# Performance work log

Measured on AMD Instinct MI355X. Metric: run time of the kernel, lower is better.

The kernel has to match this reference:

```python
import jax, jax.numpy as jnp
import numpy as np

S_IN = 32      # input spatial size
KSZ = 3        # kernel size
STRIDE = 1
S_OUT = (S_IN - KSZ) // STRIDE + 1   # 30
C_IN = 16      # input capsule types
C_OUT = 32     # output capsule types
ROUTINGS = 3
EPS = 1e-7     # K.epsilon()


def _child_parent_map(size_in, size_out, kernel_size):
    # For each parent position, the flat indices of its kernel_size^2 children.
    cpm = np.zeros((size_out ** 2, kernel_size ** 2), dtype=np.int32)
    for p in range(size_out ** 2):
        idx = []
        for kr in range(kernel_size):
            start = kr * size_in + p % size_out + (p // size_out) * size_in
            idx.extend(range(start, start + kernel_size))
        cpm[p] = idx
    return cpm

_CPM = jnp.asarray(_child_parent_map(S_IN, S_OUT, KSZ))  # [S_OUT^2, KSZ^2]


def setup_inputs() -> dict:
    key = jax.random.key(0)
    k1, k2, k3, k4, k5 = jax.random.split(key, 5)
    return {
        "input_act": jax.random.uniform(k1, (S_IN, S_IN, C_IN, 1), dtype=jnp.float32),
        "input_pose": jax.random.normal(k2, (S_IN, S_IN, C_IN, 4, 4), dtype=jnp.float32),
        "transformation_weights": jax.random.normal(k3, (1, KSZ * KSZ * C_IN, C_OUT, 4, 4), dtype=jnp.float32) * 0.1,
        "beta_a": jax.random.normal(k4, (1, 1, C_OUT), dtype=jnp.float32),
        "beta_v": jax.random.normal(k5, (1, 1, C_OUT, 1), dtype=jnp.float32),
    }


def reference(input_act, input_pose, transformation_weights, beta_a, beta_v):
    P = S_OUT ** 2                 # parent positions
    N = KSZ * KSZ * C_IN           # children per parent

    pose = input_pose.reshape(S_IN ** 2, C_IN, 4, 4)
    act = input_act.reshape(S_IN ** 2, C_IN, 1)

    # gather children per parent position (irregular gather via child_parent_map)
    pose_f = pose[_CPM].reshape(P, N, 4, 4)        # [P, N, 4, 4]
    act_f = act[_CPM].reshape(P, N, 1, 1)          # [P, N, 1, 1] (broadcasts over C_OUT)

    W = transformation_weights[0]                  # [N, C_OUT, 4, 4]
    # votes[p,n,c,i,j] = sum_k pose_f[p,n,i,k] * W[n,c,k,j] (avoids K.tile materialization)
    votes = jnp.einsum('pnik,nckj->pncij', pose_f, W).reshape(P, N, C_OUT, 16)

    rr = jnp.full((P, N, C_OUT, 1), 1.0 / C_OUT, dtype=votes.dtype)

    out_act = None
    means = None
    for i in range(ROUTINGS):
        lambd = 0.01 * (1.0 - 0.95 ** i)
        # ---- M step ----
        rs = jnp.sum(rr, axis=1, keepdims=True)                              # [P,1,C,1]
        means = jnp.sum(rr * votes, axis=1, keepdims=True) / rs              # [P,1,C,16]
        var = jnp.sum(rr * jnp.square(votes - means), axis=1, keepdims=True) / rs
        std = jnp.sqrt(var)                                                  # [P,1,C,16]
        costs = beta_v + jnp.log(std + EPS) * rs                             # [P,1,C,16]
        out_act = jax.nn.sigmoid(lambd * (beta_a - jnp.sum(costs, axis=-1)))[..., None]  # [P,1,C,1]
        if i < ROUTINGS - 1:
            # ---- E step ----
            prob_exp = -jnp.sum(jnp.square(votes - means) / (2.0 * jnp.square(std)),
                                axis=-1, keepdims=True)                      # [P,N,C,1]
            prob_main = -jnp.sum(jnp.log(std + EPS), axis=-1, keepdims=True)  # [P,1,C,1]
            zz = jnp.log(out_act + EPS) + prob_main + prob_exp
            rr = jax.nn.softmax(zz, axis=0)                                   # softmax over parent axis, as in source

    out_act = out_act.reshape(S_OUT, S_OUT, C_OUT, 1)
    out_pose = means.reshape(S_OUT, S_OUT, C_OUT, 4, 4)
    return (out_act, out_pose)
```

## Files before the change

### kernel.cpp

```cpp
#include <hip/hip_runtime.h>
#include <hip/hip_bf16.h>


#define S_IN   32
#define S_OUT  30
#define PP     (S_OUT * S_OUT)
#define NN     144
#define NPO    113
#define EPSF   1e-7f
#define CLAMPA 80.0f

template <bool FIRST, bool LAST>
__global__ __launch_bounds__(256, 2) void mstep_kernel(
    const float* __restrict__ pose,
    const float* __restrict__ W,
    const float* __restrict__ beta_a,
    const float* __restrict__ beta_v,
    const float* __restrict__ colsum,
    float* __restrict__ zero0,
    float* __restrict__ zero1,
    float* __restrict__ meanw,
    float* __restrict__ i2vw,
    float* __restrict__ basew,
    float* __restrict__ out,
    float lambd)
{
    const int p = blockIdx.x;
    const int t = threadIdx.x;
    const int c = t & 31;
    const int slot = t >> 5;
    const int wave = t >> 6;

    __shared__ float pose_s[NN * 16];
    __shared__ float red[33 * 4 * 32];

    const int prow = p / S_OUT, pcol = p % S_OUT;
    {
        const float4* pose4 = (const float4*)pose;
        float4* ps4 = (float4*)pose_s;
        for (int idx = t; idx < 576; idx += 256) {
            int kk = idx >> 6;
            int child = (prow + kk / 3) * S_IN + (pcol + kk % 3);
            ps4[idx] = pose4[child * 64 + (idx & 63)];
        }
    }
    if (FIRST) {
        if (p < 18) zero0[p * 256 + t] = 0.f;
        else if (p < 36) zero1[(p - 18) * 256 + t] = 0.f;
    }

    float mn[16], iv[16], base = 0.f;
    if (!FIRST) {
        const float4* m4 = (const float4*)&meanw[(p * 32 + c) * 16];
        const float4* v4 = (const float4*)&i2vw[(p * 32 + c) * 16];
#pragma unroll
        for (int q = 0; q < 4; ++q) {
            float4 a = m4[q], b = v4[q];
            mn[q * 4 + 0] = a.x; mn[q * 4 + 1] = a.y; mn[q * 4 + 2] = a.z; mn[q * 4 + 3] = a.w;
            iv[q * 4 + 0] = b.x; iv[q * 4 + 1] = b.y; iv[q * 4 + 2] = b.z; iv[q * 4 + 3] = b.w;
        }
        base = basew[p * 32 + c];
    }
    __syncthreads();

    float rsum = 0.f;
    float s1[16], s2[16];
#pragma unroll
    for (int q = 0; q < 16; ++q) { s1[q] = 0.f; s2[q] = 0.f; }

    float w[16];
    float cs = 1.f;
    {
        const float4* wp = (const float4*)&W[(slot * 32 + c) * 16];
        float4 w0 = wp[0], w1 = wp[1], w2 = wp[2], w3 = wp[3];
        w[0] = w0.x; w[1] = w0.y; w[2] = w0.z; w[3] = w0.w;
        w[4] = w1.x; w[5] = w1.y; w[6] = w1.z; w[7] = w1.w;
        w[8] = w2.x; w[9] = w2.y; w[10] = w2.z; w[11] = w2.w;
        w[12] = w3.x; w[13] = w3.y; w[14] = w3.z; w[15] = w3.w;
        if (!FIRST) cs = colsum[slot * 32 + c];
    }

    for (int k = 0; k < 18; ++k) {
        const int n = (k << 3) + slot;
        float4 wn0, wn1, wn2, wn3; float csn = 1.f;
        if (k < 17) {
            const float4* wp = (const float4*)&W[((n + 8) * 32 + c) * 16];
            wn0 = wp[0]; wn1 = wp[1]; wn2 = wp[2]; wn3 = wp[3];
            if (!FIRST) csn = colsum[(n + 8) * 32 + c];
        }
        const float* pr = &pose_s[n * 16];
        float v[16];
#pragma unroll
        for (int i = 0; i < 4; ++i) {
            float p0 = pr[i * 4 + 0], p1 = pr[i * 4 + 1];
            float p2 = pr[i * 4 + 2], p3 = pr[i * 4 + 3];
#pragma unroll
            for (int j = 0; j < 4; ++j)
                v[i * 4 + j] = p0 * w[j] + p1 * w[4 + j] + p2 * w[8 + j] + p3 * w[12 + j];
        }
        float r;
        if (FIRST) {
            r = 1.0f / 32.0f;
        } else {
            float pe = 0.f;
#pragma unroll
            for (int q = 0; q < 16; ++q) {
                float d = v[q] - mn[q];
                pe = fmaf(d * d, iv[q], pe);
            }
            r = __expf(fminf(base - pe, CLAMPA)) * __builtin_amdgcn_rcpf(cs);
        }
#pragma unroll
        for (int q = 0; q < 16; ++q) {
            s1[q] = fmaf(r, v[q], s1[q]);
            s2[q] = fmaf(r * v[q], v[q], s2[q]);
        }
        rsum += r;
        if (k < 17) {
            w[0] = wn0.x; w[1] = wn0.y; w[2] = wn0.z; w[3] = wn0.w;
            w[4] = wn1.x; w[5] = wn1.y; w[6] = wn1.z; w[7] = wn1.w;
            w[8] = wn2.x; w[9] = wn2.y; w[10] = wn2.z; w[11] = wn2.w;
            w[12] = wn3.x; w[13] = wn3.y; w[14] = wn3.z; w[15] = wn3.w;
            cs = csn;
        }
    }

#pragma unroll
    for (int q = 0; q < 16; ++q) {
        s1[q] += __shfl_xor(s1[q], 32);
        s2[q] += __shfl_xor(s2[q], 32);
    }
    rsum += __shfl_xor(rsum, 32);

    if ((t & 32) == 0) {
#pragma unroll
        for (int q = 0; q < 16; ++q) {
            red[(q * 4 + wave) * 32 + c] = s1[q];
            red[((16 + q) * 4 + wave) * 32 + c] = s2[q];
        }
        red[(32 * 4 + wave) * 32 + c] = rsum;
    }
    __syncthreads();

    if (t < 32) {
        float rs = 0.f;
#pragma unroll
        for (int w4 = 0; w4 < 4; ++w4) rs += red[(32 * 4 + w4) * 32 + c];
        float inv_rs = 1.0f / rs;
        float logstd_sum = 0.f;
        float mean[16], i2v[16];
#pragma unroll
        for (int q = 0; q < 16; ++q) {
            float a1 = 0.f, a2 = 0.f;
#pragma unroll
            for (int w4 = 0; w4 < 4; ++w4) {
                a1 += red[(q * 4 + w4) * 32 + c];
                a2 += red[((16 + q) * 4 + w4) * 32 + c];
            }
            float m = a1 * inv_rs;
            float var = a2 * inv_rs - m * m;
            var = fmaxf(var, 1e-30f);
            float sd = __builtin_sqrtf(var);
            mean[q] = m;
            i2v[q] = 0.5f / var;
            logstd_sum += __logf(sd + EPSF);
        }
        float sumcosts = 16.f * beta_v[c] + rs * logstd_sum;
        float a = 1.0f / (1.0f + __expf(-(lambd * (beta_a[c] - sumcosts))));
        if (LAST) {
            out[p * 32 + c] = a;
            float4* op4 = (float4*)(out + PP * 32);
#pragma unroll
            for (int q = 0; q < 4; ++q) {
                float4 vv; vv.x = mean[q * 4]; vv.y = mean[q * 4 + 1];
                vv.z = mean[q * 4 + 2]; vv.w = mean[q * 4 + 3];
                op4[(p * 32 + c) * 4 + q] = vv;
            }
        } else {
            basew[p * 32 + c] = __logf(a + EPSF) - logstd_sum;
            float4* m4 = (float4*)&meanw[(p * 32 + c) * 16];
            float4* v4 = (float4*)&i2vw[(p * 32 + c) * 16];
#pragma unroll
            for (int q = 0; q < 4; ++q) {
                float4 mv; mv.x = mean[q * 4]; mv.y = mean[q * 4 + 1];
                mv.z = mean[q * 4 + 2]; mv.w = mean[q * 4 + 3];
                float4 vv; vv.x = i2v[q * 4]; vv.y = i2v[q * 4 + 1];
                vv.z = i2v[q * 4 + 2]; vv.w = i2v[q * 4 + 3];
                m4[q] = mv; v4[q] = vv;
            }
        }
    }
}

__global__ __launch_bounds__(256, 3) void estep_kernel(
    const float* __restrict__ pose, const float* __restrict__ W,
    const float* __restrict__ meanw, const float* __restrict__ i2vw,
    const float* __restrict__ basew,
    float* __restrict__ colsum)
{
    const int b = blockIdx.x;
    const int po = b % NPO;
    const int kk = b / NPO;
    const int t = threadIdx.x;
    const int c = t & 31;
    const int ps = t >> 5;
    const int p = po * 8 + ps;
    const bool valid = p < PP;
    const int pc = valid ? p : (PP - 1);

    __shared__ float pose_s[8 * 16 * 16];
    __shared__ float zs[16 * 8 * 32];

    const int kr = kk / 3, kc = kk % 3;
    {
        const float4* pose4 = (const float4*)pose;
        float4* ps4 = (float4*)pose_s;
        for (int idx = t; idx < 512; idx += 256) {
            int pi = idx >> 6;
            int pp = po * 8 + pi;
            int ppc = pp < PP ? pp : (PP - 1);
            int child = (ppc / S_OUT + kr) * S_IN + (ppc % S_OUT + kc);
            ps4[idx] = pose4[child * 64 + (idx & 63)];
        }
    }

    float mn[16], iv[16];
    {
        const float4* m4 = (const float4*)&meanw[(pc * 32 + c) * 16];
        const float4* v4 = (const float4*)&i2vw[(pc * 32 + c) * 16];
#pragma unroll
        for (int q = 0; q < 4; ++q) {
            float4 a = m4[q], bb = v4[q];
            mn[q * 4 + 0] = a.x; mn[q * 4 + 1] = a.y; mn[q * 4 + 2] = a.z; mn[q * 4 + 3] = a.w;
            iv[q * 4 + 0] = bb.x; iv[q * 4 + 1] = bb.y; iv[q * 4 + 2] = bb.z; iv[q * 4 + 3] = bb.w;
        }
    }
    const float base = basew[pc * 32 + c];
    __syncthreads();

    float w[16];
    {
        const float4* wp = (const float4*)&W[((kk * 16) * 32 + c) * 16];
        float4 w0 = wp[0], w1 = wp[1], w2 = wp[2], w3 = wp[3];
        w[0] = w0.x; w[1] = w0.y; w[2] = w0.z; w[3] = w0.w;
        w[4] = w1.x; w[5] = w1.y; w[6] = w1.z; w[7] = w1.w;
        w[8] = w2.x; w[9] = w2.y; w[10] = w2.z; w[11] = w2.w;
        w[12] = w3.x; w[13] = w3.y; w[14] = w3.z; w[15] = w3.w;
    }

    for (int ci = 0; ci < 16; ++ci) {
        float4 wn0, wn1, wn2, wn3;
        if (ci < 15) {
            const float4* wp = (const float4*)&W[((kk * 16 + ci + 1) * 32 + c) * 16];
            wn0 = wp[0]; wn1 = wp[1]; wn2 = wp[2]; wn3 = wp[3];
        }
        const float* pr = &pose_s[(ps * 16 + ci) * 16];
        float pe = 0.f;
#pragma unroll
        for (int i = 0; i < 4; ++i) {
            float p0 = pr[i * 4 + 0], p1 = pr[i * 4 + 1];
            float p2 = pr[i * 4 + 2], p3 = pr[i * 4 + 3];
#pragma unroll
            for (int j = 0; j < 4; ++j) {
                float v = p0 * w[j] + p1 * w[4 + j] + p2 * w[8 + j] + p3 * w[12 + j];
                float d = v - mn[i * 4 + j];
                pe = fmaf(d * d, iv[i * 4 + j], pe);
            }
        }
        zs[(ci * 8 + ps) * 32 + c] = valid ? __expf(fminf(base - pe, CLAMPA)) : 0.f;
        if (ci < 15) {
            w[0] = wn0.x; w[1] = wn0.y; w[2] = wn0.z; w[3] = wn0.w;
            w[4] = wn1.x; w[5] = wn1.y; w[6] = wn1.z; w[7] = wn1.w;
            w[8] = wn2.x; w[9] = wn2.y; w[10] = wn2.z; w[11] = wn2.w;
            w[12] = wn3.x; w[13] = wn3.y; w[14] = wn3.z; w[15] = wn3.w;
        }
    }
    __syncthreads();

#pragma unroll
    for (int r = 0; r < 2; ++r) {
        const int pair = t + r * 256;
        const int ci = pair >> 5, cc = pair & 31;
        float ssum = 0.f;
#pragma unroll
        for (int s = 0; s < 8; ++s) ssum += zs[(ci * 8 + s) * 32 + cc];
        atomicAdd(&colsum[(kk * 16 + ci) * 32 + cc], ssum);
    }
}

extern "C" void kernel_launch(void* const* d_in, const int* in_sizes, int n_in,
                              void* d_out, int out_size, void* d_ws, size_t ws_size,
                              hipStream_t stream) {
    const float* pose   = (const float*)d_in[1];
    const float* W      = (const float*)d_in[2];
    const float* beta_a = (const float*)d_in[3];
    const float* beta_v = (const float*)d_in[4];
    float* out = (float*)d_out;
    float* ws = (float*)d_ws;

    float* meanw = ws;
    float* i2vw  = meanw + PP * 32 * 16;
    float* basew = i2vw + PP * 32 * 16;
    float* cs0   = basew + PP * 32;
    float* cs1   = cs0 + NN * 32;

    const float lambd0 = 0.0f;
    const float lambd1 = 0.01f * (1.0f - 0.95f);
    const float lambd2 = 0.01f * (1.0f - 0.95f * 0.95f);

    const int eg = 9 * NPO;

    mstep_kernel<true, false><<<PP, 256, 0, stream>>>(
        pose, W, beta_a, beta_v, cs0, cs0, cs1, meanw, i2vw, basew, out, lambd0);
    estep_kernel<<<eg, 256, 0, stream>>>(pose, W, meanw, i2vw, basew, cs0);
    mstep_kernel<false, false><<<PP, 256, 0, stream>>>(
        pose, W, beta_a, beta_v, cs0, cs0, cs1, meanw, i2vw, basew, out, lambd1);
    estep_kernel<<<eg, 256, 0, stream>>>(pose, W, meanw, i2vw, basew, cs1);
    mstep_kernel<false, true><<<PP, 256, 0, stream>>>(
        pose, W, beta_a, beta_v, cs1, cs0, cs1, meanw, i2vw, basew, out, lambd2);
}
```

Baseline: 137.1 us.

## Fuse E-step into M-step kernel, reusing staged pose tile and parallelizing finalize

```diff
diff --git a/kernel.cpp b/kernel.cpp
--- a/kernel.cpp
+++ b/kernel.cpp
@@ -1,24 +1,51 @@
 #include <hip/hip_runtime.h>
-#include <hip/hip_bf16.h>
 
 
 #define S_IN   32
 #define S_OUT  30
 #define PP     (S_OUT * S_OUT)
 #define NN     144
-#define NPO    113
 #define EPSF   1e-7f
 #define CLAMPA 80.0f
 
+#define LOADW(dst, n_) do {                                              \
+    const float4* _wp = (const float4*)&W[((n_) * 32 + c) * 16];         \
+    float4 _w0 = _wp[0], _w1 = _wp[1], _w2 = _wp[2], _w3 = _wp[3];       \
+    dst[0] = _w0.x; dst[1] = _w0.y; dst[2] = _w0.z; dst[3] = _w0.w;      \
+    dst[4] = _w1.x; dst[5] = _w1.y; dst[6] = _w1.z; dst[7] = _w1.w;      \
+    dst[8] = _w2.x; dst[9] = _w2.y; dst[10] = _w2.z; dst[11] = _w2.w;    \
+    dst[12] = _w3.x; dst[13] = _w3.y; dst[14] = _w3.z; dst[15] = _w3.w;  \
+} while (0)
+
+#define LOADPO(dst, n_) do {                                             \
+    const float4* _pp = (const float4*)&pose_s[(n_) * 16];               \
+    float4 _p0 = _pp[0], _p1 = _pp[1], _p2 = _pp[2], _p3 = _pp[3];       \
+    dst[0] = _p0.x; dst[1] = _p0.y; dst[2] = _p0.z; dst[3] = _p0.w;      \
+    dst[4] = _p1.x; dst[5] = _p1.y; dst[6] = _p1.z; dst[7] = _p1.w;      \
+    dst[8] = _p2.x; dst[9] = _p2.y; dst[10] = _p2.z; dst[11] = _p2.w;    \
+    dst[12] = _p3.x; dst[13] = _p3.y; dst[14] = _p3.z; dst[15] = _p3.w;  \
+} while (0)
+
+#define VOTES(v_, po_, w_) do {                                          \
+    _Pragma("unroll")                                                    \
+    for (int _i = 0; _i < 4; ++_i) {                                     \
+        float _p0 = po_[_i*4+0], _p1 = po_[_i*4+1];                      \
+        float _p2 = po_[_i*4+2], _p3 = po_[_i*4+3];                      \
+        _Pragma("unroll")                                                \
+        for (int _j = 0; _j < 4; ++_j)                                   \
+            v_[_i*4+_j] = fmaf(_p0, w_[_j], fmaf(_p1, w_[4+_j],          \
+                          fmaf(_p2, w_[8+_j], _p3 * w_[12+_j])));        \
+    }                                                                    \
+} while (0)
+
 template <bool FIRST, bool LAST>
-__global__ __launch_bounds__(256, 2) void mstep_kernel(
+__global__ __launch_bounds__(256, 4) void me_kernel(
     const float* __restrict__ pose,
     const float* __restrict__ W,
     const float* __restrict__ beta_a,
     const float* __restrict__ beta_v,
-    const float* __restrict__ colsum,
-    float* __restrict__ zero0,
-    float* __restrict__ zero1,
+    const float* __restrict__ csR,
+    float* __restrict__ csW,
     float* __restrict__ meanw,
     float* __restrict__ i2vw,
     float* __restrict__ basew,
@@ -33,6 +60,10 @@
 
     __shared__ float pose_s[NN * 16];
     __shared__ float red[33 * 4 * 32];
+    __shared__ float mean_s[32 * 16];
+    __shared__ float i2v_s[32 * 16];
+    __shared__ float base_s[32];
+    __shared__ float lg[4 * 32];
 
     const int prow = p / S_OUT, pcol = p % S_OUT;
     {
@@ -44,10 +75,6 @@
             ps4[idx] = pose4[child * 64 + (idx & 63)];
         }
     }
-    if (FIRST) {
-        if (p < 18) zero0[p * 256 + t] = 0.f;
-        else if (p < 36) zero1[(p - 18) * 256 + t] = 0.f;
-    }
 
     float mn[16], iv[16], base = 0.f;
     if (!FIRST) {
@@ -69,38 +96,27 @@
     for (int q = 0; q < 16; ++q) { s1[q] = 0.f; s2[q] = 0.f; }
 
     float w[16];
+    LOADW(w, slot);
     float cs = 1.f;
-    {
-        const float4* wp = (const float4*)&W[(slot * 32 + c) * 16];
-        float4 w0 = wp[0], w1 = wp[1], w2 = wp[2], w3 = wp[3];
-        w[0] = w0.x; w[1] = w0.y; w[2] = w0.z; w[3] = w0.w;
-        w[4] = w1.x; w[5] = w1.y; w[6] = w1.z; w[7] = w1.w;
-        w[8] = w2.x; w[9] = w2.y; w[10] = w2.z; w[11] = w2.w;
-        w[12] = w3.x; w[13] = w3.y; w[14] = w3.z; w[15] = w3.w;
-        if (!FIRST) cs = colsum[slot * 32 + c];
-    }
+    if (!FIRST) cs = csR[slot * 32 + c];
 
     for (int k = 0; k < 18; ++k) {
         const int n = (k << 3) + slot;
-        float4 wn0, wn1, wn2, wn3; float csn = 1.f;
+        float po[16];
+        LOADPO(po, n);
+        float v[16];
+        VOTES(v, po, w);
+        float cs_next = cs;
         if (k < 17) {
-            const float4* wp = (const float4*)&W[((n + 8) * 32 + c) * 16];
-            wn0 = wp[0]; wn1 = wp[1]; wn2 = wp[2]; wn3 = wp[3];
-            if (!FIRST) csn = colsum[(n + 8) * 32 + c];
-        }
-        const float* pr = &pose_s[n * 16];
-        float v[16];
-#pragma unroll
-        for (int i = 0; i < 4; ++i) {
-            float p0 = pr[i * 4 + 0], p1 = pr[i * 4 + 1];
-            float p2 = pr[i * 4 + 2], p3 = pr[i * 4 + 3];
-#pragma unroll
-            for (int j = 0; j < 4; ++j)
-                v[i * 4 + j] = p0 * w[j] + p1 * w[4 + j] + p2 * w[8 + j] + p3 * w[12 + j];
-        }
-        float r;
+            LOADW(w, n + 8);
+            if (!FIRST) cs_next = csR[(n + 8) * 32 + c];
+        }
         if (FIRST) {
-            r = 1.0f / 32.0f;
+#pragma unroll
+            for (int q = 0; q < 16; ++q) {
+                s1[q] += v[q];
+                s2[q] = fmaf(v[q], v[q], s2[q]);
+            }
         } else {
             float pe = 0.f;
 #pragma unroll
@@ -108,21 +124,16 @@
                 float d = v[q] - mn[q];
                 pe = fmaf(d * d, iv[q], pe);
             }
-            r = __expf(fminf(base - pe, CLAMPA)) * __builtin_amdgcn_rcpf(cs);
-        }
-#pragma unroll
-        for (int q = 0; q < 16; ++q) {
-            s1[q] = fmaf(r, v[q], s1[q]);
-            s2[q] = fmaf(r * v[q], v[q], s2[q]);
-        }
-        rsum += r;
-        if (k < 17) {
-            w[0] = wn0.x; w[1] = wn0.y; w[2] = wn0.z; w[3] = wn0.w;
-            w[4] = wn1.x; w[5] = wn1.y; w[6] = wn1.z; w[7] = wn1.w;
-            w[8] = wn2.x; w[9] = wn2.y; w[10] = wn2.z; w[11] = wn2.w;
-            w[12] = wn3.x; w[13] = wn3.y; w[14] = wn3.z; w[15] = wn3.w;
-            cs = csn;
-        }
+            float r = __expf(fminf(base - pe, CLAMPA)) * __builtin_amdgcn_rcpf(cs);
+#pragma unroll
+            for (int q = 0; q < 16; ++q) {
+                s1[q] = fmaf(r, v[q], s1[q]);
+                float rv = r * v[q];
+                s2[q] = fmaf(rv, v[q], s2[q]);
+            }
+            rsum += r;
+        }
+        cs = cs_next;
     }
 
 #pragma unroll
@@ -142,149 +153,93 @@
     }
     __syncthreads();
 
+    if (t < 128) {
+        const int qq = t >> 5, cl = t & 31;
+        float rs, inv_rs;
+        if (FIRST) {
+            rs = 4.5f;
+            inv_rs = 1.0f / 144.0f;
+        } else {
+            rs = red[(32 * 4 + 0) * 32 + cl] + red[(32 * 4 + 1) * 32 + cl] +
+                 red[(32 * 4 + 2) * 32 + cl] + red[(32 * 4 + 3) * 32 + cl];
+            inv_rs = 1.0f / rs;
+        }
+        float lsum = 0.f;
+        float mq[4], vq[4];
+#pragma unroll
+        for (int u = 0; u < 4; ++u) {
+            const int q = qq * 4 + u;
+            float a1 = red[(q * 4 + 0) * 32 + cl] + red[(q * 4 + 1) * 32 + cl] +
+                       red[(q * 4 + 2) * 32 + cl] + red[(q * 4 + 3) * 32 + cl];
+            float a2 = red[((16 + q) * 4 + 0) * 32 + cl] + red[((16 + q) * 4 + 1) * 32 + cl] +
+                       red[((16 + q) * 4 + 2) * 32 + cl] + red[((16 + q) * 4 + 3) * 32 + cl];
+            float m = a1 * inv_rs;
+            float var = fmaxf(a2 * inv_rs - m * m, 1e-30f);
+            float sd = __builtin_sqrtf(var);
+            mq[u] = m;
+            vq[u] = 0.5f / var;
+            lsum += __logf(sd + EPSF);
+            mean_s[cl * 16 + q] = m;
+            i2v_s[cl * 16 + q] = vq[u];
+        }
+        lg[qq * 32 + cl] = lsum;
+        float4 mv; mv.x = mq[0]; mv.y = mq[1]; mv.z = mq[2]; mv.w = mq[3];
+        if (LAST) {
+            ((float4*)(out + PP * 32))[(p * 32 + cl) * 4 + qq] = mv;
+        } else {
+            float4 vv; vv.x = vq[0]; vv.y = vq[1]; vv.z = vq[2]; vv.w = vq[3];
+            ((float4*)meanw)[(p * 32 + cl) * 4 + qq] = mv;
+            ((float4*)i2vw)[(p * 32 + cl) * 4 + qq] = vv;
+        }
+    }
+    __syncthreads();
+
     if (t < 32) {
-        float rs = 0.f;
-#pragma unroll
-        for (int w4 = 0; w4 < 4; ++w4) rs += red[(32 * 4 + w4) * 32 + c];
-        float inv_rs = 1.0f / rs;
-        float logstd_sum = 0.f;
-        float mean[16], i2v[16];
-#pragma unroll
-        for (int q = 0; q < 16; ++q) {
-            float a1 = 0.f, a2 = 0.f;
-#pragma unroll
-            for (int w4 = 0; w4 < 4; ++w4) {
-                a1 += red[(q * 4 + w4) * 32 + c];
-                a2 += red[((16 + q) * 4 + w4) * 32 + c];
-            }
-            float m = a1 * inv_rs;
-            float var = a2 * inv_rs - m * m;
-            var = fmaxf(var, 1e-30f);
-            float sd = __builtin_sqrtf(var);
-            mean[q] = m;
-            i2v[q] = 0.5f / var;
-            logstd_sum += __logf(sd + EPSF);
-        }
-        float sumcosts = 16.f * beta_v[c] + rs * logstd_sum;
+        float rs = FIRST ? 4.5f
+                 : red[(32 * 4 + 0) * 32 + c] + red[(32 * 4 + 1) * 32 + c] +
+                   red[(32 * 4 + 2) * 32 + c] + red[(32 * 4 + 3) * 32 + c];
+        float lsum = lg[c] + lg[32 + c] + lg[64 + c] + lg[96 + c];
+        float sumcosts = 16.f * beta_v[c] + rs * lsum;
         float a = 1.0f / (1.0f + __expf(-(lambd * (beta_a[c] - sumcosts))));
         if (LAST) {
             out[p * 32 + c] = a;
-            float4* op4 = (float4*)(out + PP * 32);
+        } else {
+            float b = __logf(a + EPSF) - lsum;
+            basew[p * 32 + c] = b;
+            base_s[c] = b;
+        }
+    }
+
+    if (!LAST) {
+        __syncthreads();
+        float tbase = base_s[c];
+        {
+            const float4* m4 = (const float4*)&mean_s[c * 16];
+            const float4* v4 = (const float4*)&i2v_s[c * 16];
 #pragma unroll
             for (int q = 0; q < 4; ++q) {
-                float4 vv; vv.x = mean[q * 4]; vv.y = mean[q * 4 + 1];
-                vv.z = mean[q * 4 + 2]; vv.w = mean[q * 4 + 3];
-                op4[(p * 32 + c) * 4 + q] = vv;
-            }
-        } else {
-            basew[p * 32 + c] = __logf(a + EPSF) - logstd_sum;
-            float4* m4 = (float4*)&meanw[(p * 32 + c) * 16];
-            float4* v4 = (float4*)&i2vw[(p * 32 + c) * 16];
-#pragma unroll
-            for (int q = 0; q < 4; ++q) {
-                float4 mv; mv.x = mean[q * 4]; mv.y = mean[q * 4 + 1];
-                mv.z = mean[q * 4 + 2]; mv.w = mean[q * 4 + 3];
-                float4 vv; vv.x = i2v[q * 4]; vv.y = i2v[q * 4 + 1];
-                vv.z = i2v[q * 4 + 2]; vv.w = i2v[q * 4 + 3];
-                m4[q] = mv; v4[q] = vv;
-            }
-        }
-    }
-}
-
-__global__ __launch_bounds__(256, 3) void estep_kernel(
-    const float* __restrict__ pose, const float* __restrict__ W,
-    const float* __restrict__ meanw, const float* __restrict__ i2vw,
-    const float* __restrict__ basew,
-    float* __restrict__ colsum)
-{
-    const int b = blockIdx.x;
-    const int po = b % NPO;
-    const int kk = b / NPO;
-    const int t = threadIdx.x;
-    const int c = t & 31;
-    const int ps = t >> 5;
-    const int p = po * 8 + ps;
-    const bool valid = p < PP;
-    const int pc = valid ? p : (PP - 1);
-
-    __shared__ float pose_s[8 * 16 * 16];
-    __shared__ float zs[16 * 8 * 32];
-
-    const int kr = kk / 3, kc = kk % 3;
-    {
-        const float4* pose4 = (const float4*)pose;
-        float4* ps4 = (float4*)pose_s;
-        for (int idx = t; idx < 512; idx += 256) {
-            int pi = idx >> 6;
-            int pp = po * 8 + pi;
-            int ppc = pp < PP ? pp : (PP - 1);
-            int child = (ppc / S_OUT + kr) * S_IN + (ppc % S_OUT + kc);
-            ps4[idx] = pose4[child * 64 + (idx & 63)];
-        }
-    }
-
-    float mn[16], iv[16];
-    {
-        const float4* m4 = (const float4*)&meanw[(pc * 32 + c) * 16];
-        const float4* v4 = (const float4*)&i2vw[(pc * 32 + c) * 16];
-#pragma unroll
-        for (int q = 0; q < 4; ++q) {
-            float4 a = m4[q], bb = v4[q];
-            mn[q * 4 + 0] = a.x; mn[q * 4 + 1] = a.y; mn[q * 4 + 2] = a.z; mn[q * 4 + 3] = a.w;
-            iv[q * 4 + 0] = bb.x; iv[q * 4 + 1] = bb.y; iv[q * 4 + 2] = bb.z; iv[q * 4 + 3] = bb.w;
-        }
-    }
-    const float base = basew[pc * 32 + c];
-    __syncthreads();
-
-    float w[16];
-    {
-        const float4* wp = (const float4*)&W[((kk * 16) * 32 + c) * 16];
-        float4 w0 = wp[0], w1 = wp[1], w2 = wp[2], w3 = wp[3];
-        w[0] = w0.x; w[1] = w0.y; w[2] = w0.z; w[3] = w0.w;
-        w[4] = w1.x; w[5] = w1.y; w[6] = w1.z; w[7] = w1.w;
-        w[8] = w2.x; w[9] = w2.y; w[10] = w2.z; w[11] = w2.w;
-        w[12] = w3.x; w[13] = w3.y; w[14] = w3.z; w[15] = w3.w;
-    }
-
-    for (int ci = 0; ci < 16; ++ci) {
-        float4 wn0, wn1, wn2, wn3;
-        if (ci < 15) {
-            const float4* wp = (const float4*)&W[((kk * 16 + ci + 1) * 32 + c) * 16];
-            wn0 = wp[0]; wn1 = wp[1]; wn2 = wp[2]; wn3 = wp[3];
-        }
-        const float* pr = &pose_s[(ps * 16 + ci) * 16];
-        float pe = 0.f;
-#pragma unroll
-        for (int i = 0; i < 4; ++i) {
-            float p0 = pr[i * 4 + 0], p1 = pr[i * 4 + 1];
-            float p2 = pr[i * 4 + 2], p3 = pr[i * 4 + 3];
-#pragma unroll
-            for (int j = 0; j < 4; ++j) {
-                float v = p0 * w[j] + p1 * w[4 + j] + p2 * w[8 + j] + p3 * w[12 + j];
-                float d = v - mn[i * 4 + j];
-                pe = fmaf(d * d, iv[i * 4 + j], pe);
-            }
-        }
-        zs[(ci * 8 + ps) * 32 + c] = valid ? __expf(fminf(base - pe, CLAMPA)) : 0.f;
-        if (ci < 15) {
-            w[0] = wn0.x; w[1] = wn0.y; w[2] = wn0.z; w[3] = wn0.w;
-            w[4] = wn1.x; w[5] = wn1.y; w[6] = wn1.z; w[7] = wn1.w;
-            w[8] = wn2.x; w[9] = wn2.y; w[10] = wn2.z; w[11] = wn2.w;
-            w[12] = wn3.x; w[13] = wn3.y; w[14] = wn3.z; w[15] = wn3.w;
-        }
-    }
-    __syncthreads();
-
-#pragma unroll
-    for (int r = 0; r < 2; ++r) {
-        const int pair = t + r * 256;
-        const int ci = pair >> 5, cc = pair & 31;
-        float ssum = 0.f;
-#pragma unroll
-        for (int s = 0; s < 8; ++s) ssum += zs[(ci * 8 + s) * 32 + cc];
-        atomicAdd(&colsum[(kk * 16 + ci) * 32 + cc], ssum);
+                float4 a = m4[q], b = v4[q];
+                mn[q * 4 + 0] = a.x; mn[q * 4 + 1] = a.y; mn[q * 4 + 2] = a.z; mn[q * 4 + 3] = a.w;
+                iv[q * 4 + 0] = b.x; iv[q * 4 + 1] = b.y; iv[q * 4 + 2] = b.z; iv[q * 4 + 3] = b.w;
+            }
+        }
+        LOADW(w, slot);
+        for (int k = 0; k < 18; ++k) {
+            const int n = (k << 3) + slot;
+            float po[16];
+            LOADPO(po, n);
+            float v[16];
+            VOTES(v, po, w);
+            if (k < 17) LOADW(w, n + 8);
+            float pe = 0.f;
+#pragma unroll
+            for (int q = 0; q < 16; ++q) {
+                float d = v[q] - mn[q];
+                pe = fmaf(d * d, iv[q], pe);
+            }
+            float e = __expf(fminf(tbase - pe, CLAMPA));
+            atomicAdd(&csW[n * 32 + c], e);
+        }
     }
 }
 
@@ -308,14 +263,12 @@
     const float lambd1 = 0.01f * (1.0f - 0.95f);
     const float lambd2 = 0.01f * (1.0f - 0.95f * 0.95f);
 
-    const int eg = 9 * NPO;
-
-    mstep_kernel<true, false><<<PP, 256, 0, stream>>>(
-        pose, W, beta_a, beta_v, cs0, cs0, cs1, meanw, i2vw, basew, out, lambd0);
-    estep_kernel<<<eg, 256, 0, stream>>>(pose, W, meanw, i2vw, basew, cs0);
-    mstep_kernel<false, false><<<PP, 256, 0, stream>>>(
-        pose, W, beta_a, beta_v, cs0, cs0, cs1, meanw, i2vw, basew, out, lambd1);
-    estep_kernel<<<eg, 256, 0, stream>>>(pose, W, meanw, i2vw, basew, cs1);
-    mstep_kernel<false, true><<<PP, 256, 0, stream>>>(
-        pose, W, beta_a, beta_v, cs1, cs0, cs1, meanw, i2vw, basew, out, lambd2);
+    hipMemsetAsync(cs0, 0, 2 * NN * 32 * sizeof(float), stream);
+
+    me_kernel<true, false><<<PP, 256, 0, stream>>>(
+        pose, W, beta_a, beta_v, cs0, cs0, meanw, i2vw, basew, out, lambd0);
+    me_kernel<false, false><<<PP, 256, 0, stream>>>(
+        pose, W, beta_a, beta_v, cs0, cs1, meanw, i2vw, basew, out, lambd1);
+    me_kernel<false, true><<<PP, 256, 0, stream>>>(
+        pose, W, beta_a, beta_v, cs1, nullptr, meanw, i2vw, basew, out, lambd2);
 }
```

Result: slower. 170.2 us (+24.1%).
